# Performance work log

Hardware: AMD Instinct MI355X
Metric: run time of the kernel (lower is better)

Reference implementation:

```python
import jax, jax.numpy as jnp
import numpy as np

DIM = 256
NUM_HEADS = 8
HEAD_DIM = DIM // NUM_HEADS
Z_SHAPE = (32, 32)   # template grid -> qL = 1024
X_SHAPE = (64, 64)   # search grid  -> kvL = 4096
TBL = (max(Z_SHAPE[0], X_SHAPE[0]), max(Z_SHAPE[1], X_SHAPE[1]))  # (64, 64)
N_TABLE = (2 * TBL[0] - 1) * (2 * TBL[1] - 1)  # 16129


def _make_rel_index():
    """Faithful replication of the torch module's buffer construction (numpy, vectorized)."""
    H, W = TBL
    coords = np.stack(np.meshgrid(np.arange(H), np.arange(W), indexing='ij'), 0).reshape(2, -1)
    rel = coords[:, :, None] - coords[:, None, :]                     # (2, HW, HW)
    idx = (rel[0] + H - 1) * (2 * W - 1) + (rel[1] + W - 1)           # (HW, HW)
    h_z_begin = int(H / 2 - Z_SHAPE[0] / 2); h_x_begin = int(H / 2 - X_SHAPE[0] / 2)
    w_z_begin = int(W / 2 - Z_SHAPE[1] / 2); w_x_begin = int(W / 2 - X_SHAPE[1] / 2)
    hz = np.arange(h_z_begin, h_z_begin + Z_SHAPE[0])
    hx = np.arange(h_x_begin, h_x_begin + X_SHAPE[0])
    wz = np.arange(w_z_begin, w_z_begin + Z_SHAPE[1])
    wx = np.arange(w_x_begin, w_x_begin + X_SHAPE[1])
    # NOTE: source multiplies by z_2d_shape[0]/z_2d_shape[1] (kept faithfully, even though it looks odd)
    z_pos = hz[:, None] * Z_SHAPE[0] + wz[None, :]                    # (32, 32) axes (h_z, w_z)
    x_pos = hx[:, None] * Z_SHAPE[1] + wx[None, :]                    # (64, 64) axes (h_x, w_x)
    g = idx[z_pos][:, :, x_pos]                                       # (h_z, w_z, h_x, w_x)
    g = g.transpose(0, 2, 1, 3).reshape(Z_SHAPE[0] * Z_SHAPE[1], X_SHAPE[0] * X_SHAPE[1])
    return jnp.asarray(g, dtype=jnp.int32)                           # (qL, kvL)


def setup_inputs() -> dict:
    key = jax.random.key(0)
    ks = jax.random.split(key, 10)
    B, qL, kvL, C = 4, Z_SHAPE[0] * Z_SHAPE[1], X_SHAPE[0] * X_SHAPE[1], DIM
    return {
        'q': jax.random.normal(ks[0], (B, qL, C), jnp.float32),
        'kv': jax.random.normal(ks[1], (B, kvL, C), jnp.float32),
        'Wq': jax.random.normal(ks[2], (C, C), jnp.float32) * 0.02,
        'bq': jnp.zeros((C,), jnp.float32),
        'Wkv': jax.random.normal(ks[3], (2 * C, C), jnp.float32) * 0.02,
        'bkv': jnp.zeros((2 * C,), jnp.float32),
        'bias_table': jax.random.normal(ks[4], (N_TABLE, NUM_HEADS), jnp.float32) * 0.02,
        'Wp': jax.random.normal(ks[5], (C, C), jnp.float32) * 0.02,
        'bp': jnp.zeros((C,), jnp.float32),
        'rel_index': _make_rel_index(),
    }


def reference(q, kv, Wq, bq, Wkv, bkv, bias_table, Wp, bp, rel_index):
    B, qL, C = q.shape
    kvL = kv.shape[1]
    H, hd = NUM_HEADS, HEAD_DIM
    scale = hd ** (-0.5)
    Q = (q @ Wq.T + bq).reshape(B, qL, H, hd) * scale                  # bqhd
    KV = (kv @ Wkv.T + bkv).reshape(B, kvL, 2, H, hd)
    K, V = KV[:, :, 0], KV[:, :, 1]                                    # bkhd
    attn = jnp.einsum('bqhd,bkhd->bhqk', Q, K)                         # (B,H,qL,kvL)
    bias = bias_table[rel_index]                                       # (qL,kvL,H)
    attn = attn + jnp.transpose(bias, (2, 0, 1))[None]
    attn = jax.nn.softmax(attn, axis=-1)
    x = jnp.einsum('bhqk,bkhd->bqhd', attn, V).reshape(B, qL, C)
    return x @ Wp.T + bp
```

## Files before the change

kernel.cpp:

```cpp
#include <hip/hip_runtime.h>
#include <math.h>

#define DIM 256
#define NUM_HEADS 8
#define HEAD_DIM 32
#define QL 1024
#define KVL 4096
#define BATCH 4
#define NTAB 16129
#define LOG2E 1.4426950408889634f

typedef __attribute__((ext_vector_type(8))) short short8;
typedef __attribute__((ext_vector_type(4))) float floatx4;
typedef __attribute__((ext_vector_type(4))) unsigned short ushort4v;

__device__ inline unsigned short f2bf(float x) {
    unsigned u = __builtin_bit_cast(unsigned, x);
    unsigned r = (u + 0x7FFFu + ((u >> 16) & 1u)) >> 16;
    return (unsigned short)r;
}
__device__ inline float bf2f(unsigned short h) {
    return __builtin_bit_cast(float, (unsigned)h << 16);
}
__device__ inline floatx4 mfma16(short8 a, short8 b, floatx4 c) {
    return __builtin_amdgcn_mfma_f32_16x16x32_bf16(a, b, c, 0, 0, 0);
}

__global__ __launch_bounds__(256) void split_all(
    const float* __restrict__ q, const float* __restrict__ kv,
    const float* __restrict__ Wq, const float* __restrict__ Wkv,
    const float* __restrict__ Wp, const float* __restrict__ bias_table,
    unsigned short* __restrict__ qh, unsigned short* __restrict__ kvh,
    unsigned short* __restrict__ Wqh, unsigned short* __restrict__ Wkvh,
    unsigned short* __restrict__ Wph, unsigned short* __restrict__ Wpl,
    float* __restrict__ Bt)
{
    const int gid = blockIdx.x * 256 + threadIdx.x;
    if (gid >= 1408514) return;
    if (gid >= 1376256) {
        const int local = gid - 1376256;
        const float4 v = ((const float4*)bias_table)[local];
        const float vv[4] = {v.x, v.y, v.z, v.w};
        const int base = local * 4;
#pragma unroll
        for (int j = 0; j < 4; ++j) {
            const int i = (base + j) >> 3, h = (base + j) & 7;
            Bt[h * NTAB + i] = vv[j] * LOG2E;
        }
        return;
    }
    const float* src; unsigned short* dh; unsigned short* dl = nullptr; int local;
    if (gid < 262144)       { src = q;   dh = qh;   local = gid; }
    else if (gid < 1310720) { src = kv;  dh = kvh;  local = gid - 262144; }
    else if (gid < 1327104) { src = Wq;  dh = Wqh;  local = gid - 1310720; }
    else if (gid < 1359872) { src = Wkv; dh = Wkvh; local = gid - 1327104; }
    else                    { src = Wp;  dh = Wph;  dl = Wpl; local = gid - 1359872; }
    const float4 v = ((const float4*)src)[local];
    ushort4v h;
    h[0] = f2bf(v.x); h[1] = f2bf(v.y); h[2] = f2bf(v.z); h[3] = f2bf(v.w);
    ((ushort4v*)dh)[local] = h;
    if (dl) {
        ushort4v l;
        l[0] = f2bf(v.x - bf2f(h[0])); l[1] = f2bf(v.y - bf2f(h[1]));
        l[2] = f2bf(v.z - bf2f(h[2])); l[3] = f2bf(v.w - bf2f(h[3]));
        ((ushort4v*)dl)[local] = l;
    }
}

template<int MODE, int BW>
__device__ __forceinline__ void gemm_core(
    const unsigned short* __restrict__ Ah, const unsigned short* __restrict__ Al,
    const unsigned short* __restrict__ Wh, const unsigned short* __restrict__ Wl,
    const float* __restrict__ bias, float* __restrict__ Cf,
    unsigned short* __restrict__ Cb, float scale, int bx, int by)
{
    constexpr bool THREE = (MODE == 0);
    const int t    = threadIdx.x;
    const int w    = t >> 6;
    const int lane = t & 63;
    const int n16  = lane & 15;
    const int quad = lane >> 4;
    const int m0 = by * (BW * 32) + w * 32;
    const int n0 = bx * 64;

    floatx4 acc[2][4];
#pragma unroll
    for (int s = 0; s < 2; ++s)
#pragma unroll
        for (int c = 0; c < 4; ++c) acc[s][c] = (floatx4){0.f, 0.f, 0.f, 0.f};

    short8 af[2][2], afl[2][2], wf[2][4], wfl[2][4];

    auto LD = [&](int kb, int bi) {
#pragma unroll
        for (int s = 0; s < 2; ++s) {
            af[bi][s] = *(const short8*)(Ah + (size_t)(m0 + s * 16 + n16) * 256 + kb + quad * 8);
            if (THREE)
                afl[bi][s] = *(const short8*)(Al + (size_t)(m0 + s * 16 + n16) * 256 + kb + quad * 8);
        }
#pragma unroll
        for (int c = 0; c < 4; ++c) {
            wf[bi][c] = *(const short8*)(Wh + (size_t)(n0 + c * 16 + n16) * 256 + kb + quad * 8);
            if (THREE)
                wfl[bi][c] = *(const short8*)(Wl + (size_t)(n0 + c * 16 + n16) * 256 + kb + quad * 8);
        }
    };

    LD(0, 0);
#pragma unroll
    for (int i = 0; i < 8; ++i) {
        const int cur = i & 1, nxt = cur ^ 1;
        if (i < 7) LD((i + 1) * 32, nxt);
#pragma unroll
        for (int c = 0; c < 4; ++c)
#pragma unroll
            for (int s = 0; s < 2; ++s) {
                acc[s][c] = mfma16(af[cur][s], wf[cur][c], acc[s][c]);
                if (THREE) {
                    acc[s][c] = mfma16(af[cur][s], wfl[cur][c], acc[s][c]);
                    acc[s][c] = mfma16(afl[cur][s], wf[cur][c], acc[s][c]);
                }
            }
    }

#pragma unroll
    for (int s = 0; s < 2; ++s)
#pragma unroll
        for (int c = 0; c < 4; ++c) {
            const floatx4 v = acc[s][c];
            const int n_g = n0 + c * 16 + n16;
#pragma unroll
            for (int r = 0; r < 4; ++r) {
                const int m_g = m0 + s * 16 + quad * 4 + r;
                const float val = v[r];
                if (MODE == 0) {
                    Cf[(size_t)m_g * 256 + n_g] = val + bias[n_g];
                } else if (MODE == 1) {
                    const int h = n_g >> 5, d = n_g & 31;
                    const int b = m_g >> 10, qq = m_g & 1023;
                    Cb[(((size_t)(b * 8 + h) * 1024 + qq) << 5) + d] =
                        f2bf((val + bias[n_g]) * scale);
                } else if (MODE == 2) {
                    const int h = n_g >> 5, d = n_g & 31;
                    const int b = m_g >> 12, kvr = m_g & 4095;
                    Cb[(((size_t)(b * 8 + h) * 4096 + kvr) << 5) + d] =
                        f2bf(val + bias[n_g]);
                } else {
                    const int h = m_g >> 5, dd = m_g & 31;
                    const int b = n_g >> 12, kvr = n_g & 4095;
                    Cb[(((size_t)((b * 8 + h) * 32 + dd)) << 12) + kvr] =
                        f2bf(val + bias[m_g]);
                }
            }
        }
}

__global__ __launch_bounds__(256) void gemm_qkv(
    const unsigned short* __restrict__ qh, const unsigned short* __restrict__ kvh,
    const unsigned short* __restrict__ Wqh, const unsigned short* __restrict__ Wkvh,
    const float* __restrict__ bq, const float* __restrict__ bkv,
    unsigned short* __restrict__ Qb, unsigned short* __restrict__ Kb,
    unsigned short* __restrict__ Vt, float scale)
{
    const int id = blockIdx.x;
    if (id < 128) {
        gemm_core<1, 4>(qh, nullptr, Wqh, nullptr, bq, nullptr, Qb, scale,
                        id & 3, id >> 2);
    } else if (id < 640) {
        const int t2 = id - 128;
        gemm_core<2, 4>(kvh, nullptr, Wkvh, nullptr, bkv, nullptr, Kb, 1.0f,
                        t2 & 3, t2 >> 2);
    } else {
        const int t2 = id - 640;
        gemm_core<3, 4>(Wkvh + 256 * 256, nullptr, kvh, nullptr, bkv + 256,
                        nullptr, Vt, 1.0f, t2 >> 1, t2 & 1);
    }
}

__global__ __launch_bounds__(128) void gemm_out(
    const unsigned short* __restrict__ Xh, const unsigned short* __restrict__ Xl,
    const unsigned short* __restrict__ Wph, const unsigned short* __restrict__ Wpl,
    const float* __restrict__ bp, float* __restrict__ out)
{
    gemm_core<0, 2>(Xh, Xl, Wph, Wpl, bp, out, nullptr, 1.0f,
                    blockIdx.x, blockIdx.y);
}

__global__ __launch_bounds__(256, 3) void attn_mfma(
    const unsigned short* __restrict__ Qb,
    const unsigned short* __restrict__ Kb,
    const unsigned short* __restrict__ Vt,
    const float* __restrict__ Bt,
    float* __restrict__ Op,
    float* __restrict__ lp)
{
    const int id   = blockIdx.x;
    const int qt   = id >> 7;
    const int rest = id & 127;
    const int h    = rest & 7;
    const int sp   = (rest >> 3) & 3;
    const int b    = rest >> 5;
    const int bh = b * NUM_HEADS + h;
    const int tid  = threadIdx.x;
    const int w    = tid >> 6;
    const int lane = tid & 63;
    const int n    = lane & 15;
    const int quad = lane >> 4;

    __shared__ __align__(16) unsigned short Ps[4][16 * 72];

    const int qrowA = qt * 64 + w * 16 + n;
    const short8 qf = *(const short8*)(Qb + (((size_t)bh * QL + qrowA) << 5) + quad * 8);

    const int qgC = qt * 64 + w * 16 + quad * 4;
    const float* Bth = Bt + h * NTAB;

    const int vS = sp >> 1;
    int ivals[4], B0r[4];
#pragma unroll
    for (int r = 0; r < 4; ++r) {
        const int q = qgC + r;
        ivals[r] = q >> 5;
        B0r[r]   = (((q & 31) << 1) + vS) << 5;
    }

    floatx4 o0 = {0.f, 0.f, 0.f, 0.f};
    floatx4 o1 = {0.f, 0.f, 0.f, 0.f};
    float lacc[4] = {0.f, 0.f, 0.f, 0.f};

    const unsigned short* Kbase = Kb + (((size_t)bh * KVL) << 5);
    const unsigned short* Vbase = Vt + (((size_t)bh * 32) << 12);
    const int kbase = sp * 1024;

    short8 kf[2][4];
    float  bv[2][16];

    auto LDK = [&](int kt, int bi) {
        const int kv0 = kbase + kt * 64;
#pragma unroll
        for (int c = 0; c < 4; ++c)
            kf[bi][c] = *(const short8*)(Kbase + ((size_t)(kv0 + c * 16 + n) << 5) + quad * 8);
    };
    auto GATHER = [&](int kt, int bi) {
        const int jS = ((sp << 4) + kt) & 31;
#pragma unroll
        for (int r = 0; r < 4; ++r) {
            const int a  = 528 + (ivals[r] << 5) + jS;
            const int A0 = ((a >> 6) + 63) * 127 + (a & 63) + 63;
#pragma unroll
            for (int c = 0; c < 4; ++c) {
                const int bb  = B0r[r] + c * 16 + n;
                const int idx = A0 - ((bb >> 6) * 127 + (bb & 63));
                bv[bi][r * 4 + c] = Bth[idx];
            }
        }
    };

    LDK(0, 0);
    GATHER(0, 0);

#pragma unroll
    for (int kt = 0; kt < 16; ++kt) {
        const int cur = kt & 1, nxt = cur ^ 1;
        const int kv0 = kbase + kt * 64;

        short8 vf[2][2];
#pragma unroll
        for (int kc = 0; kc < 2; ++kc)
#pragma unroll
            for (int dh = 0; dh < 2; ++dh)
                vf[kc][dh] = *(const short8*)(Vbase + ((size_t)(dh * 16 + n) << 12)
                                              + kv0 + kc * 32 + quad * 8);

        floatx4 sc[4];
#pragma unroll
        for (int c = 0; c < 4; ++c) {
            floatx4 z = {0.f, 0.f, 0.f, 0.f};
            sc[c] = mfma16(qf, kf[cur][c], z);
        }

        if (kt < 15) { LDK(kt + 1, nxt); GATHER(kt + 1, nxt); }

#pragma unroll
        for (int r = 0; r < 4; ++r)
#pragma unroll
            for (int c = 0; c < 4; ++c) {
                const float p = exp2f(fmaf(sc[c][r], LOG2E, bv[cur][r * 4 + c]));
                lacc[r] += p;
                Ps[w][(quad * 4 + r) * 72 + c * 16 + n] = f2bf(p);
            }
        asm volatile("s_waitcnt lgkmcnt(0)" ::: "memory");

#pragma unroll
        for (int kc = 0; kc < 2; ++kc) {
            const short8 pf = *(const short8*)(Ps[w] + n * 72 + kc * 32 + quad * 8);
            o0 = mfma16(pf, vf[kc][0], o0);
            o1 = mfma16(pf, vf[kc][1], o1);
        }
        asm volatile("" ::: "memory");
    }

#pragma unroll
    for (int r = 0; r < 4; ++r) {
        float v = lacc[r];
        v += __shfl_xor(v, 1, 16);
        v += __shfl_xor(v, 2, 16);
        v += __shfl_xor(v, 4, 16);
        v += __shfl_xor(v, 8, 16);
        lacc[r] = v;
    }

    float* Opb = Op + (((size_t)(sp * 32 + bh) * QL) << 5);
#pragma unroll
    for (int r = 0; r < 4; ++r) {
        const int qg = qgC + r;
        Opb[((size_t)qg << 5) + n]      = o0[r];
        Opb[((size_t)qg << 5) + 16 + n] = o1[r];
    }
    if (n == 0) {
        float* lpb = lp + (size_t)(sp * 32 + bh) * QL;
#pragma unroll
        for (int r = 0; r < 4; ++r) lpb[qgC + r] = lacc[r];
    }
}

__global__ __launch_bounds__(256) void attn_combine(
    const float* __restrict__ Op, const float* __restrict__ lp,
    unsigned short* __restrict__ Xh, unsigned short* __restrict__ Xl)
{
    const int gid = blockIdx.x * 256 + threadIdx.x;
    const int bhq = gid >> 5, d = gid & 31;
    const int bh = bhq >> 10, q = bhq & 1023;
    const int b = bh >> 3, hh = bh & 7;
    float o = 0.f, l = 0.f;
#pragma unroll
    for (int s = 0; s < 4; ++s) {
        o += Op[((size_t)(s * 32768 + bhq) << 5) + d];
        l += lp[s * 32768 + bhq];
    }
    const float val = o / l;
    const size_t idx = ((size_t)(b * QL + q)) * DIM + hh * HEAD_DIM + d;
    const unsigned short h = f2bf(val);
    Xh[idx] = h;
    Xl[idx] = f2bf(val - bf2f(h));
}

extern "C" void kernel_launch(void* const* d_in, const int* in_sizes, int n_in,
                              void* d_out, int out_size, void* d_ws, size_t ws_size,
                              hipStream_t stream)
{
    const float* q          = (const float*)d_in[0];
    const float* kv         = (const float*)d_in[1];
    const float* Wq         = (const float*)d_in[2];
    const float* bq         = (const float*)d_in[3];
    const float* Wkv        = (const float*)d_in[4];
    const float* bkv        = (const float*)d_in[5];
    const float* bias_table = (const float*)d_in[6];
    const float* Wp         = (const float*)d_in[7];
    const float* bp         = (const float*)d_in[8];
    float* out = (float*)d_out;

    char* ws = (char*)d_ws;
    unsigned short* Qb   = (unsigned short*)(ws);
    unsigned short* Kb   = (unsigned short*)(ws + (size_t)(2u  << 20));
    unsigned short* Vt   = (unsigned short*)(ws + (size_t)(10u << 20));
    unsigned short* kvh  = (unsigned short*)(ws + (size_t)(18u << 20));
    float*          Op   = (float*)         (ws + (size_t)(18u << 20));
    float*          lp   = (float*)         (ws + (size_t)(34u << 20));
    float*          Bt   = (float*)         (ws + (size_t)(34u << 20) + (512u << 10));
    unsigned short* qh   = (unsigned short*)(ws + (size_t)(36u << 20));
    unsigned short* Wqh  = (unsigned short*)(ws + (size_t)(38u << 20));
    unsigned short* Wkvh = (unsigned short*)(ws + (size_t)(38u << 20) + (128u << 10));
    unsigned short* Wph  = (unsigned short*)(ws + (size_t)(38u << 20) + (384u << 10));
    unsigned short* Wpl  = (unsigned short*)(ws + (size_t)(38u << 20) + (512u << 10));
    unsigned short* Xh   = qh;
    unsigned short* Xl   = Vt;

    const float scale = 1.0f / sqrtf((float)HEAD_DIM);

    split_all<<<dim3(5503), 256, 0, stream>>>(q, kv, Wq, Wkv, Wp, bias_table,
                                              qh, kvh, Wqh, Wkvh, Wph, Wpl, Bt);
    gemm_qkv<<<dim3(1152), 256, 0, stream>>>(qh, kvh, Wqh, Wkvh, bq, bkv,
                                             Qb, Kb, Vt, scale);
    attn_mfma<<<dim3(2048), 256, 0, stream>>>(Qb, Kb, Vt, Bt, Op, lp);
    attn_combine<<<dim3(4096), 256, 0, stream>>>(Op, lp, Xh, Xl);
    gemm_out<<<dim3(4, 64), 128, 0, stream>>>(Xh, Xl, Wph, Wpl, bp, out);
}
```

Baseline: 246.1 us.

## Transpose MFMA operand order so each lane owns a query row, vectorizing bias gathers and stores

Swaps the A/B operands of both MFMAs so the accumulator holds scores transposed: each lane now owns one query row and four consecutive kv positions. This turns the 16 scalar bias-table gathers per tile into four 4-wide loads of contiguous table entries read in reversed order. It also lets P be written to LDS as packed 4-element stores and output be written as float4. The row-sum reduction becomes a two-step cross-quad shuffle instead of four shuffles per row. The unaligned float4 gathers rely on the table index decreasing by exactly one across consecutive kv positions within a chunk.

```diff
diff --git a/kernel.cpp b/kernel.cpp
--- a/kernel.cpp
+++ b/kernel.cpp
@@ -13,6 +13,7 @@
 typedef __attribute__((ext_vector_type(8))) short short8;
 typedef __attribute__((ext_vector_type(4))) float floatx4;
 typedef __attribute__((ext_vector_type(4))) unsigned short ushort4v;
+typedef float float4a __attribute__((ext_vector_type(4), aligned(4)));
 
 __device__ inline unsigned short f2bf(float x) {
     unsigned u = __builtin_bit_cast(unsigned, x);
@@ -209,31 +210,31 @@
 
     __shared__ __align__(16) unsigned short Ps[4][16 * 72];
 
-    const int qrowA = qt * 64 + w * 16 + n;
-    const short8 qf = *(const short8*)(Qb + (((size_t)bh * QL + qrowA) << 5) + quad * 8);
-
-    const int qgC = qt * 64 + w * 16 + quad * 4;
+    const int qrow = qt * 64 + w * 16 + n;
+    const short8 qf = *(const short8*)(Qb + (((size_t)bh * QL + qrow) << 5) + quad * 8);
+
     const float* Bth = Bt + h * NTAB;
-
     const int vS = sp >> 1;
-    int ivals[4], B0r[4];
-#pragma unroll
-    for (int r = 0; r < 4; ++r) {
-        const int q = qgC + r;
-        ivals[r] = q >> 5;
-        B0r[r]   = (((q & 31) << 1) + vS) << 5;
+
+    const int iq = qrow >> 5, uq = qrow & 31;
+    const int B0 = ((uq << 1) + vS) << 5;
+    int Moff[4];
+#pragma unroll
+    for (int c = 0; c < 4; ++c) {
+        const int bb = B0 + c * 16 + quad * 4;
+        Moff[c] = (bb >> 6) * 127 + (bb & 63);
     }
 
     floatx4 o0 = {0.f, 0.f, 0.f, 0.f};
     floatx4 o1 = {0.f, 0.f, 0.f, 0.f};
-    float lacc[4] = {0.f, 0.f, 0.f, 0.f};
+    float lacc = 0.f;
 
     const unsigned short* Kbase = Kb + (((size_t)bh * KVL) << 5);
     const unsigned short* Vbase = Vt + (((size_t)bh * 32) << 12);
     const int kbase = sp * 1024;
 
-    short8 kf[2][4];
-    float  bv[2][16];
+    short8  kf[2][4];
+    float4a bfv[2][4];
 
     auto LDK = [&](int kt, int bi) {
         const int kv0 = kbase + kt * 64;
@@ -243,17 +244,11 @@
     };
     auto GATHER = [&](int kt, int bi) {
         const int jS = ((sp << 4) + kt) & 31;
-#pragma unroll
-        for (int r = 0; r < 4; ++r) {
-            const int a  = 528 + (ivals[r] << 5) + jS;
-            const int A0 = ((a >> 6) + 63) * 127 + (a & 63) + 63;
-#pragma unroll
-            for (int c = 0; c < 4; ++c) {
-                const int bb  = B0r[r] + c * 16 + n;
-                const int idx = A0 - ((bb >> 6) * 127 + (bb & 63));
-                bv[bi][r * 4 + c] = Bth[idx];
-            }
-        }
+        const int a  = 528 + (iq << 5) + jS;
+        const int A0 = ((a >> 6) + 63) * 127 + (a & 63) + 63;
+#pragma unroll
+        for (int c = 0; c < 4; ++c)
+            bfv[bi][c] = *(const float4a*)(Bth + (A0 - Moff[c] - 3));
     };
 
     LDK(0, 0);
@@ -276,52 +271,42 @@
 #pragma unroll
         for (int c = 0; c < 4; ++c) {
             floatx4 z = {0.f, 0.f, 0.f, 0.f};
-            sc[c] = mfma16(qf, kf[cur][c], z);
+            sc[c] = mfma16(kf[cur][c], qf, z);
         }
 
         if (kt < 15) { LDK(kt + 1, nxt); GATHER(kt + 1, nxt); }
 
 #pragma unroll
-        for (int r = 0; r < 4; ++r)
-#pragma unroll
-            for (int c = 0; c < 4; ++c) {
-                const float p = exp2f(fmaf(sc[c][r], LOG2E, bv[cur][r * 4 + c]));
-                lacc[r] += p;
-                Ps[w][(quad * 4 + r) * 72 + c * 16 + n] = f2bf(p);
+        for (int c = 0; c < 4; ++c) {
+            ushort4v pk;
+#pragma unroll
+            for (int r = 0; r < 4; ++r) {
+                const float p = exp2f(fmaf(sc[c][r], LOG2E, bfv[cur][c][3 - r]));
+                lacc += p;
+                pk[r] = f2bf(p);
             }
+            *(ushort4v*)(Ps[w] + n * 72 + c * 16 + quad * 4) = pk;
+        }
         asm volatile("s_waitcnt lgkmcnt(0)" ::: "memory");
 
 #pragma unroll
         for (int kc = 0; kc < 2; ++kc) {
             const short8 pf = *(const short8*)(Ps[w] + n * 72 + kc * 32 + quad * 8);
-            o0 = mfma16(pf, vf[kc][0], o0);
-            o1 = mfma16(pf, vf[kc][1], o1);
+            o0 = mfma16(vf[kc][0], pf, o0);
+            o1 = mfma16(vf[kc][1], pf, o1);
         }
         asm volatile("" ::: "memory");
     }
 
-#pragma unroll
-    for (int r = 0; r < 4; ++r) {
-        float v = lacc[r];
-        v += __shfl_xor(v, 1, 16);
-        v += __shfl_xor(v, 2, 16);
-        v += __shfl_xor(v, 4, 16);
-        v += __shfl_xor(v, 8, 16);
-        lacc[r] = v;
-    }
+    lacc += __shfl_xor(lacc, 16, 64);
+    lacc += __shfl_xor(lacc, 32, 64);
 
     float* Opb = Op + (((size_t)(sp * 32 + bh) * QL) << 5);
-#pragma unroll
-    for (int r = 0; r < 4; ++r) {
-        const int qg = qgC + r;
-        Opb[((size_t)qg << 5) + n]      = o0[r];
-        Opb[((size_t)qg << 5) + 16 + n] = o1[r];
-    }
-    if (n == 0) {
-        float* lpb = lp + (size_t)(sp * 32 + bh) * QL;
-#pragma unroll
-        for (int r = 0; r < 4; ++r) lpb[qgC + r] = lacc[r];
-    }
+    const int qg = qt * 64 + w * 16 + n;
+    *(floatx4*)(Opb + ((size_t)qg << 5) + quad * 4)      = o0;
+    *(floatx4*)(Opb + ((size_t)qg << 5) + 16 + quad * 4) = o1;
+    if (quad == 0)
+        lp[(size_t)(sp * 32 + bh) * QL + qg] = lacc;
 }
 
 __global__ __launch_bounds__(256) void attn_combine(
```

Result: slower. 286.1 us (+16.2%).

## Process two query subtiles per wave and inline bias gather in attention

Applied to the files above, without the earlier changes.

The attention kernel now uses 128-thread blocks, with each wave handling 32 query rows as two 16-row subtiles. Each K/V fragment load is therefore reused across twice as many MFMAs. The bias gather is no longer double-buffered in registers and is loaded inline right before use. exp2f is replaced by raw v_exp_f32, and bf16 rounding becomes a cheaper round-half-up conversion. This cuts per-element ALU and global-load overhead, at the cost of exposing gather latency, fewer waves per block, and a slightly different rounding mode.

```diff
diff --git a/kernel.cpp b/kernel.cpp
--- a/kernel.cpp
+++ b/kernel.cpp
@@ -19,8 +19,16 @@
     unsigned r = (u + 0x7FFFu + ((u >> 16) & 1u)) >> 16;
     return (unsigned short)r;
 }
+__device__ inline unsigned short f2bf_fast(float x) {
+    return (unsigned short)((__builtin_bit_cast(unsigned, x) + 0x8000u) >> 16);
+}
 __device__ inline float bf2f(unsigned short h) {
     return __builtin_bit_cast(float, (unsigned)h << 16);
+}
+__device__ inline float fast_exp2(float x) {
+    float r;
+    asm("v_exp_f32 %0, %1" : "=v"(r) : "v"(x));
+    return r;
 }
 __device__ inline floatx4 mfma16(short8 a, short8 b, floatx4 c) {
     return __builtin_amdgcn_mfma_f32_16x16x32_bf16(a, b, c, 0, 0, 0);
@@ -186,7 +194,7 @@
                     blockIdx.x, blockIdx.y);
 }
 
-__global__ __launch_bounds__(256, 3) void attn_mfma(
+__global__ __launch_bounds__(128, 4) void attn_mfma(
     const unsigned short* __restrict__ Qb,
     const unsigned short* __restrict__ Kb,
     const unsigned short* __restrict__ Vt,
@@ -207,62 +215,54 @@
     const int n    = lane & 15;
     const int quad = lane >> 4;
 
-    __shared__ __align__(16) unsigned short Ps[4][16 * 72];
-
-    const int qrowA = qt * 64 + w * 16 + n;
-    const short8 qf = *(const short8*)(Qb + (((size_t)bh * QL + qrowA) << 5) + quad * 8);
-
-    const int qgC = qt * 64 + w * 16 + quad * 4;
+    __shared__ __align__(16) unsigned short Ps[2][32 * 72];
+
+    short8 qf[2];
+#pragma unroll
+    for (int s = 0; s < 2; ++s) {
+        const int qrowA = qt * 64 + w * 32 + s * 16 + n;
+        qf[s] = *(const short8*)(Qb + (((size_t)bh * QL + qrowA) << 5) + quad * 8);
+    }
+
     const float* Bth = Bt + h * NTAB;
-
     const int vS = sp >> 1;
-    int ivals[4], B0r[4];
-#pragma unroll
-    for (int r = 0; r < 4; ++r) {
-        const int q = qgC + r;
-        ivals[r] = q >> 5;
-        B0r[r]   = (((q & 31) << 1) + vS) << 5;
-    }
-
-    floatx4 o0 = {0.f, 0.f, 0.f, 0.f};
-    floatx4 o1 = {0.f, 0.f, 0.f, 0.f};
-    float lacc[4] = {0.f, 0.f, 0.f, 0.f};
+
+    int ivals[2][4], B0r[2][4];
+#pragma unroll
+    for (int s = 0; s < 2; ++s)
+#pragma unroll
+        for (int r = 0; r < 4; ++r) {
+            const int q = qt * 64 + w * 32 + s * 16 + quad * 4 + r;
+            ivals[s][r] = q >> 5;
+            B0r[s][r]   = (((q & 31) << 1) + vS) << 5;
+        }
+
+    floatx4 o[2][2];
+#pragma unroll
+    for (int s = 0; s < 2; ++s)
+#pragma unroll
+        for (int dh = 0; dh < 2; ++dh) o[s][dh] = (floatx4){0.f, 0.f, 0.f, 0.f};
+    float lacc[2][4] = {};
 
     const unsigned short* Kbase = Kb + (((size_t)bh * KVL) << 5);
     const unsigned short* Vbase = Vt + (((size_t)bh * 32) << 12);
     const int kbase = sp * 1024;
 
     short8 kf[2][4];
-    float  bv[2][16];
-
     auto LDK = [&](int kt, int bi) {
         const int kv0 = kbase + kt * 64;
 #pragma unroll
         for (int c = 0; c < 4; ++c)
             kf[bi][c] = *(const short8*)(Kbase + ((size_t)(kv0 + c * 16 + n) << 5) + quad * 8);
     };
-    auto GATHER = [&](int kt, int bi) {
-        const int jS = ((sp << 4) + kt) & 31;
-#pragma unroll
-        for (int r = 0; r < 4; ++r) {
-            const int a  = 528 + (ivals[r] << 5) + jS;
-            const int A0 = ((a >> 6) + 63) * 127 + (a & 63) + 63;
-#pragma unroll
-            for (int c = 0; c < 4; ++c) {
-                const int bb  = B0r[r] + c * 16 + n;
-                const int idx = A0 - ((bb >> 6) * 127 + (bb & 63));
-                bv[bi][r * 4 + c] = Bth[idx];
-            }
-        }
-    };
 
     LDK(0, 0);
-    GATHER(0, 0);
 
 #pragma unroll
     for (int kt = 0; kt < 16; ++kt) {
         const int cur = kt & 1, nxt = cur ^ 1;
         const int kv0 = kbase + kt * 64;
+        const int jS  = ((sp << 4) + kt) & 31;
 
         short8 vf[2][2];
 #pragma unroll
@@ -272,55 +272,71 @@
                 vf[kc][dh] = *(const short8*)(Vbase + ((size_t)(dh * 16 + n) << 12)
                                               + kv0 + kc * 32 + quad * 8);
 
-        floatx4 sc[4];
-#pragma unroll
-        for (int c = 0; c < 4; ++c) {
-            floatx4 z = {0.f, 0.f, 0.f, 0.f};
-            sc[c] = mfma16(qf, kf[cur][c], z);
-        }
-
-        if (kt < 15) { LDK(kt + 1, nxt); GATHER(kt + 1, nxt); }
-
-#pragma unroll
-        for (int r = 0; r < 4; ++r)
+        if (kt < 15) LDK(kt + 1, nxt);
+
+#pragma unroll
+        for (int s = 0; s < 2; ++s) {
+            floatx4 sc[4];
 #pragma unroll
             for (int c = 0; c < 4; ++c) {
-                const float p = exp2f(fmaf(sc[c][r], LOG2E, bv[cur][r * 4 + c]));
-                lacc[r] += p;
-                Ps[w][(quad * 4 + r) * 72 + c * 16 + n] = f2bf(p);
+                floatx4 z = {0.f, 0.f, 0.f, 0.f};
+                sc[c] = mfma16(qf[s], kf[cur][c], z);
             }
+#pragma unroll
+            for (int r = 0; r < 4; ++r) {
+                const int a  = 528 + (ivals[s][r] << 5) + jS;
+                const int A0 = ((a >> 6) + 63) * 127 + (a & 63) + 63;
+#pragma unroll
+                for (int c = 0; c < 4; ++c) {
+                    const int bb  = B0r[s][r] + c * 16 + n;
+                    const int idx = A0 - ((bb >> 6) * 127 + (bb & 63));
+                    const float p = fast_exp2(fmaf(sc[c][r], LOG2E, Bth[idx]));
+                    lacc[s][r] += p;
+                    Ps[w][(s * 16 + quad * 4 + r) * 72 + c * 16 + n] = f2bf_fast(p);
+                }
+            }
+        }
         asm volatile("s_waitcnt lgkmcnt(0)" ::: "memory");
 
 #pragma unroll
-        for (int kc = 0; kc < 2; ++kc) {
-            const short8 pf = *(const short8*)(Ps[w] + n * 72 + kc * 32 + quad * 8);
-            o0 = mfma16(pf, vf[kc][0], o0);
-            o1 = mfma16(pf, vf[kc][1], o1);
-        }
+        for (int s = 0; s < 2; ++s)
+#pragma unroll
+            for (int kc = 0; kc < 2; ++kc) {
+                const short8 pf = *(const short8*)(Ps[w] + (s * 16 + n) * 72
+                                                   + kc * 32 + quad * 8);
+                o[s][0] = mfma16(pf, vf[kc][0], o[s][0]);
+                o[s][1] = mfma16(pf, vf[kc][1], o[s][1]);
+            }
         asm volatile("" ::: "memory");
     }
 
 #pragma unroll
-    for (int r = 0; r < 4; ++r) {
-        float v = lacc[r];
-        v += __shfl_xor(v, 1, 16);
-        v += __shfl_xor(v, 2, 16);
-        v += __shfl_xor(v, 4, 16);
-        v += __shfl_xor(v, 8, 16);
-        lacc[r] = v;
-    }
+    for (int s = 0; s < 2; ++s)
+#pragma unroll
+        for (int r = 0; r < 4; ++r) {
+            float v = lacc[s][r];
+            v += __shfl_xor(v, 1, 16);
+            v += __shfl_xor(v, 2, 16);
+            v += __shfl_xor(v, 4, 16);
+            v += __shfl_xor(v, 8, 16);
+            lacc[s][r] = v;
+        }
 
     float* Opb = Op + (((size_t)(sp * 32 + bh) * QL) << 5);
 #pragma unroll
-    for (int r = 0; r < 4; ++r) {
-        const int qg = qgC + r;
-        Opb[((size_t)qg << 5) + n]      = o0[r];
-        Opb[((size_t)qg << 5) + 16 + n] = o1[r];
-    }
-    if (n == 0) {
-        float* lpb = lp + (size_t)(sp * 32 + bh) * QL;
-#pragma unroll
-        for (int r = 0; r < 4; ++r) lpb[qgC + r] = lacc[r];
+    for (int s = 0; s < 2; ++s) {
+        const int qgC = qt * 64 + w * 32 + s * 16 + quad * 4;
+#pragma unroll
+        for (int r = 0; r < 4; ++r) {
+            const int qg = qgC + r;
+            Opb[((size_t)qg << 5) + n]      = o[s][0][r];
+            Opb[((size_t)qg << 5) + 16 + n] = o[s][1][r];
+        }
+        if (n == 0) {
+            float* lpb = lp + (size_t)(sp * 32 + bh) * QL;
+#pragma unroll
+            for (int r = 0; r < 4; ++r) lpb[qgC + r] = lacc[s][r];
+        }
     }
 }
 
@@ -382,7 +398,7 @@
                                               qh, kvh, Wqh, Wkvh, Wph, Wpl, Bt);
     gemm_qkv<<<dim3(1152), 256, 0, stream>>>(qh, kvh, Wqh, Wkvh, bq, bkv,
                                              Qb, Kb, Vt, scale);
-    attn_mfma<<<dim3(2048), 256, 0, stream>>>(Qb, Kb, Vt, Bt, Op, lp);
+    attn_mfma<<<dim3(2048), 128, 0, stream>>>(Qb, Kb, Vt, Bt, Op, lp);
     attn_combine<<<dim3(4096), 256, 0, stream>>>(Op, lp, Xh, Xl);
     gemm_out<<<dim3(4, 64), 128, 0, stream>>>(Xh, Xl, Wph, Wpl, bp, out);
 }
```

Result: slower. 490.1 us (+99.1%).

## Software-pipeline PV matmul one tile behind softmax; use fast exp2 and bf16 rounding

Applied to the files above, without the earlier changes.

Double-buffers the per-wave P tile in LDS and the V fragments in registers so that the P·V MFMAs for tile kt-1 are issued after the exponentials of tile kt. This removes the LDS write-then-read stall inside each iteration. It also swaps exp2f for the raw v_exp_f32 instruction and uses a simpler round-half-up bf16 conversion, which cuts VALU work. The cost is more registers and LDS, a small change in rounding behaviour, and an epilogue that drains the last tile.

```diff
diff --git a/kernel.cpp b/kernel.cpp
--- a/kernel.cpp
+++ b/kernel.cpp
@@ -19,8 +19,16 @@
     unsigned r = (u + 0x7FFFu + ((u >> 16) & 1u)) >> 16;
     return (unsigned short)r;
 }
+__device__ inline unsigned short f2bf_fast(float x) {
+    return (unsigned short)((__builtin_bit_cast(unsigned, x) + 0x8000u) >> 16);
+}
 __device__ inline float bf2f(unsigned short h) {
     return __builtin_bit_cast(float, (unsigned)h << 16);
+}
+__device__ inline float fast_exp2(float x) {
+    float r;
+    asm("v_exp_f32 %0, %1" : "=v"(r) : "v"(x));
+    return r;
 }
 __device__ inline floatx4 mfma16(short8 a, short8 b, floatx4 c) {
     return __builtin_amdgcn_mfma_f32_16x16x32_bf16(a, b, c, 0, 0, 0);
@@ -207,7 +215,7 @@
     const int n    = lane & 15;
     const int quad = lane >> 4;
 
-    __shared__ __align__(16) unsigned short Ps[4][16 * 72];
+    __shared__ __align__(16) unsigned short Ps[4][2][16 * 72];
 
     const int qrowA = qt * 64 + w * 16 + n;
     const short8 qf = *(const short8*)(Qb + (((size_t)bh * QL + qrowA) << 5) + quad * 8);
@@ -234,6 +242,7 @@
 
     short8 kf[2][4];
     float  bv[2][16];
+    short8 vf[2][2][2];
 
     auto LDK = [&](int kt, int bi) {
         const int kv0 = kbase + kt * 64;
@@ -264,13 +273,12 @@
         const int cur = kt & 1, nxt = cur ^ 1;
         const int kv0 = kbase + kt * 64;
 
-        short8 vf[2][2];
 #pragma unroll
         for (int kc = 0; kc < 2; ++kc)
 #pragma unroll
             for (int dh = 0; dh < 2; ++dh)
-                vf[kc][dh] = *(const short8*)(Vbase + ((size_t)(dh * 16 + n) << 12)
-                                              + kv0 + kc * 32 + quad * 8);
+                vf[cur][kc][dh] = *(const short8*)(Vbase + ((size_t)(dh * 16 + n) << 12)
+                                                   + kv0 + kc * 32 + quad * 8);
 
         floatx4 sc[4];
 #pragma unroll
@@ -279,25 +287,40 @@
             sc[c] = mfma16(qf, kf[cur][c], z);
         }
 
+        short8 pf0, pf1;
+        if (kt > 0) {
+            asm volatile("s_waitcnt lgkmcnt(0)" ::: "memory");
+            pf0 = *(const short8*)(Ps[w][nxt] + n * 72 + quad * 8);
+            pf1 = *(const short8*)(Ps[w][nxt] + n * 72 + 32 + quad * 8);
+        }
+
         if (kt < 15) { LDK(kt + 1, nxt); GATHER(kt + 1, nxt); }
 
 #pragma unroll
         for (int r = 0; r < 4; ++r)
 #pragma unroll
             for (int c = 0; c < 4; ++c) {
-                const float p = exp2f(fmaf(sc[c][r], LOG2E, bv[cur][r * 4 + c]));
+                const float p = fast_exp2(fmaf(sc[c][r], LOG2E, bv[cur][r * 4 + c]));
                 lacc[r] += p;
-                Ps[w][(quad * 4 + r) * 72 + c * 16 + n] = f2bf(p);
+                Ps[w][cur][(quad * 4 + r) * 72 + c * 16 + n] = f2bf_fast(p);
             }
+
+        if (kt > 0) {
+            o0 = mfma16(pf0, vf[nxt][0][0], o0);
+            o1 = mfma16(pf0, vf[nxt][0][1], o1);
+            o0 = mfma16(pf1, vf[nxt][1][0], o0);
+            o1 = mfma16(pf1, vf[nxt][1][1], o1);
+        }
+    }
+
+    {
         asm volatile("s_waitcnt lgkmcnt(0)" ::: "memory");
-
-#pragma unroll
-        for (int kc = 0; kc < 2; ++kc) {
-            const short8 pf = *(const short8*)(Ps[w] + n * 72 + kc * 32 + quad * 8);
-            o0 = mfma16(pf, vf[kc][0], o0);
-            o1 = mfma16(pf, vf[kc][1], o1);
-        }
-        asm volatile("" ::: "memory");
+        const short8 pf0 = *(const short8*)(Ps[w][1] + n * 72 + quad * 8);
+        const short8 pf1 = *(const short8*)(Ps[w][1] + n * 72 + 32 + quad * 8);
+        o0 = mfma16(pf0, vf[1][0][0], o0);
+        o1 = mfma16(pf0, vf[1][0][1], o1);
+        o0 = mfma16(pf1, vf[1][1][0], o0);
+        o1 = mfma16(pf1, vf[1][1][1], o1);
     }
 
 #pragma unroll
```

Result: slower. 252.6 us (+2.6%).
